# Optimization experiments

Measured on AMD Instinct MI355X. Metric: run time of the kernel, lower is better.

## Reference

```python
import jax, jax.numpy as jnp
import numpy as np
import math

SHIFTS = (1, 2, 4, 8)
EPS_IN = 1e-5  # InstanceNorm2d eps
EPS_BN = 1e-5  # BatchNorm2d eps

def _eight_shifts(x, d):
    # Reproduces DATrans.feature_padding: 8 reflection-padded shifted views.
    H, W = x.shape[-2], x.shape[-1]
    def p(rt, rb, cl, cr):
        return jnp.pad(x, ((0, 0), (0, 0), (rt, rb), (cl, cr)), mode='reflect')
    return [
        p(d, 0, d, 0)[..., :H, :W],   # left-top
        p(d, 0, 0, 0)[..., :H, :],    # center-top
        p(d, 0, 0, d)[..., :H, d:],   # right-top
        p(0, 0, d, 0)[..., :, :W],    # left-center
        p(0, 0, 0, d)[..., :, d:],    # right-center
        p(0, d, d, 0)[..., d:, :W],   # left-bottom
        p(0, d, 0, 0)[..., d:, :],    # center-bottom
        p(0, d, 0, d)[..., d:, d:],   # right-bottom
    ]

def _l2n(x):
    # torch F.normalize(dim=-1, eps=1e-12)
    return x / jnp.maximum(jnp.linalg.norm(x, axis=-1, keepdims=True), 1e-12)

def setup_inputs() -> dict:
    key = jax.random.key(0)
    ks = jax.random.split(key, 9)
    B, Cin, H, W = 4, 16, 256, 256
    heads, hidden, NL, Cout = 4, 16, 8, 16
    tra = heads * hidden
    cen = jax.random.normal(ks[0], (B, Cin, H, W), jnp.float32)
    q_w = jax.random.normal(ks[1], (heads, hidden, Cin), jnp.float32) / np.sqrt(Cin).astype(np.float32)
    k_w = jax.random.normal(ks[2], (heads, hidden * NL, Cin * NL), jnp.float32) / np.sqrt(Cin * NL).astype(np.float32)
    v_w = jax.random.normal(ks[3], (heads, hidden * NL, Cin * NL), jnp.float32) / np.sqrt(Cin * NL).astype(np.float32)
    out_w = jax.random.normal(ks[4], (Cout, tra), jnp.float32) / np.sqrt(tra).astype(np.float32)
    bn_gamma = jax.random.uniform(ks[5], (Cout,), jnp.float32) + 0.5
    bn_beta = jax.random.normal(ks[6], (Cout,), jnp.float32) * 0.1
    bn_mean = jax.random.normal(ks[7], (Cout,), jnp.float32) * 0.1
    bn_var = jax.random.uniform(ks[8], (Cout,), jnp.float32) + 0.5
    return dict(cen=cen, q_w=q_w, k_w=k_w, v_w=v_w, out_w=out_w,
                bn_gamma=bn_gamma, bn_beta=bn_beta, bn_mean=bn_mean, bn_var=bn_var)

def reference(cen, q_w, k_w, v_w, out_w, bn_gamma, bn_beta, bn_mean, bn_var):
    b, Cin, H, W = cen.shape
    area = H * W
    heads = len(SHIFTS)
    qs, ksl, vsl = [], [], []
    for i, d in enumerate(SHIFTS):  # small fixed loop over heads
        sur = jnp.concatenate([s - cen for s in _eight_shifts(cen, d)], axis=1)  # [b, 8*Cin, H, W]
        ksl.append(jnp.einsum('oc,bchw->bohw', k_w[i], sur))  # 1x1 conv, no bias
        vsl.append(jnp.einsum('oc,bchw->bohw', v_w[i], sur))
        qs.append(jnp.einsum('oc,bchw->bohw', q_w[i], cen))
    # torch stack(dim=2).view(b, heads, -1, area) on contiguous tensor == stack+reshape
    K = jnp.stack(ksl, axis=2).reshape(b, heads, -1, area)  # [b, heads, 8*hid, area]
    Q = jnp.stack(qs, axis=2).reshape(b, heads, -1, area)   # [b, heads, hid, area]
    V = jnp.stack(vsl, axis=2).reshape(b, heads, -1, area)
    scores = jnp.einsum('bhca,bhda->bhcd', _l2n(Q), _l2n(K)) / math.sqrt(area)  # [b,h,hid,8*hid]
    # InstanceNorm2d(heads): per (b, head) over last two dims, no affine
    mu = scores.mean(axis=(-2, -1), keepdims=True)
    var = scores.var(axis=(-2, -1), keepdims=True)
    attn = jax.nn.softmax((scores - mu) * jax.lax.rsqrt(var + EPS_IN), axis=-1)
    out = jnp.einsum('bhcd,bhda->bhca', attn, V)  # [b, heads, hid, area]
    tra = out.shape[1] * out.shape[2]
    out = out.reshape(b, tra, H, W)
    out = jnp.einsum('oc,bchw->bohw', out_w, out)  # out_conv 1x1, no bias
    g = bn_gamma[None, :, None, None]
    bta = bn_beta[None, :, None, None]
    m = bn_mean[None, :, None, None]
    v = bn_var[None, :, None, None]
    out = (out - m) * jax.lax.rsqrt(v + EPS_BN) * g + bta  # eval-mode BatchNorm2d
    return jax.nn.relu(out)
```

## Files before the change

kernel.cpp:

```cpp
#include <hip/hip_runtime.h>
#include <math.h>

#define HH 256
#define WW 256
#define AREA 65536
#define CIN 16
#define NS 4
#define CSUR 128
#define NEXT 144
#define NPAIR 45

typedef __attribute__((ext_vector_type(8))) _Float16 f16x8;
typedef __attribute__((ext_vector_type(4))) float f32x4;

__constant__ int c_dy[8] = {-1,-1,-1, 0, 0, 1, 1, 1};
__constant__ int c_dx[8] = {-1, 0, 1,-1, 1,-1, 0, 1};

__device__ constexpr int CTI[NPAIR] = {
    0, 1,1, 2,2,2, 3,3,3,3, 4,4,4,4,4,
    5,5,5,5,5,5, 6,6,6,6,6,6,6, 7,7,7,7,7,7,7,7,
    8,8,8,8,8,8,8,8,8};
__device__ constexpr int CTJ[NPAIR] = {
    0, 0,1, 0,1,2, 0,1,2,3, 0,1,2,3,4,
    0,1,2,3,4,5, 0,1,2,3,4,5,6, 0,1,2,3,4,5,6,7,
    0,1,2,3,4,5,6,7,8};

__device__ __forceinline__ int refl(int v) {
    return v < 0 ? -v : (v > 255 ? 510 - v : v);
}

__device__ __forceinline__ unsigned pkh(float a, float b) {
    auto h2 = __builtin_amdgcn_cvt_pkrtz(a, b);
    return __builtin_bit_cast(unsigned, h2);
}

__device__ __forceinline__ void wph(unsigned* __restrict__ m,
                                    int c, int pxp, int halfk, float a, float b) {
    const int sw = c & 7, gi = halfk * 4 + (pxp >> 2), e = pxp & 3;
    m[c * 32 + ((gi ^ sw) << 2) + e] = pkh(a, b);
}

template <bool FAST>
__device__ __forceinline__ void stage64(unsigned* __restrict__ m,
                                        const float* __restrict__ base,
                                        int y, int x0, int cin, int pxp, int d) {
    constexpr int DY[8] = {-1,-1,-1, 0, 0, 1, 1, 1};
    constexpr int DX[8] = {-1, 0, 1,-1, 1,-1, 0, 1};
    const int xA = x0 + 2 * pxp;
    const int xB = xA + 32;
    const float* rowy = base + y * WW;
    const float2 cA = *(const float2*)(rowy + xA);
    const float2 cB = *(const float2*)(rowy + xB);
    wph(m, cin, pxp, 0, cA.x, cA.y);
    wph(m, cin, pxp, 1, cB.x, cB.y);
#pragma unroll
    for (int kk = 0; kk < 8; ++kk) {
        float2 sA, sB;
        if (FAST) {
            const float* row = base + (y + DY[kk] * d) * WW;
            sA = *(const float2*)(row + xA + DX[kk] * d);
            sB = *(const float2*)(row + xB + DX[kk] * d);
        } else {
            const int ys = refl(y + DY[kk] * d);
            const float* row = base + ys * WW;
            const int off = DX[kk] * d;
            sA.x = row[refl(xA + off)];
            sA.y = row[refl(xA + 1 + off)];
            sB.x = row[refl(xB + off)];
            sB.y = row[refl(xB + 1 + off)];
        }
        const int c = 16 + kk * 16 + cin;
        wph(m, c, pxp, 0, sA.x - cA.x, sA.y - cA.y);
        wph(m, c, pxp, 1, sB.x - cB.x, sB.y - cB.y);
    }
}

__global__ __launch_bounds__(256) void k1_gram(const float* __restrict__ cen,
                                               float* __restrict__ part) {
    const int chunk = blockIdx.x;
    const int s = blockIdx.y;
    const int b = blockIdx.z;
    const int d = 1 << s;
    const int t = threadIdx.x;
    const int lane = t & 63, wid = t >> 6;
    const int lr = lane & 15, lg = lane >> 4;
    const int cin = t >> 4, pxp = t & 15;
    const int y0 = chunk * 4;
    const float* base = cen + ((size_t)b * CIN + cin) * AREA;

    __shared__ unsigned lds[NEXT * 32];

    const int rA = ((lg ^ (lr & 7)) << 2);
    const int rB = (((4 + lg) ^ (lr & 7)) << 2);

    f32x4 acc[12];
#pragma unroll
    for (int i = 0; i < 12; ++i) acc[i] = (f32x4){0.f, 0.f, 0.f, 0.f};

    for (int rd = 0; rd < 16; ++rd) {
        const int y  = y0 + (rd >> 2);
        const int x0 = (rd & 3) * 64;
        if (y >= 8 && y <= 247 && x0 >= 64 && x0 <= 128)
            stage64<true>(lds, base, y, x0, cin, pxp, d);
        else
            stage64<false>(lds, base, y, x0, cin, pxp, d);
        __syncthreads();
        f16x8 fA[9], fB[9];
#pragma unroll
        for (int tt = 0; tt < 9; ++tt) {
            const int rb = (tt * 16 + lr) * 32;
            fA[tt] = __builtin_bit_cast(f16x8, *(const uint4*)(lds + rb + rA));
            fB[tt] = __builtin_bit_cast(f16x8, *(const uint4*)(lds + rb + rB));
        }
        __syncthreads();
#pragma unroll
        for (int p = 0; p < NPAIR; ++p) {
            if ((p & 3) == wid) {
                const int i = CTI[p], j = CTJ[p], a = p >> 2;
                acc[a] = __builtin_amdgcn_mfma_f32_16x16x32_f16(fA[i], fA[j], acc[a], 0, 0, 0);
                acc[a] = __builtin_amdgcn_mfma_f32_16x16x32_f16(fB[i], fB[j], acc[a], 0, 0, 0);
            }
        }
    }

    float* tb = part + (size_t)((chunk & 3) * 16 + b * 4 + s) * 20736;
#pragma unroll
    for (int p = 0; p < NPAIR; ++p) {
        if ((p & 3) == wid) {
            const int gi0 = CTI[p] * 16 + lg * 4;
            const int gj  = CTJ[p] * 16 + lr;
            const f32x4 a = acc[p >> 2];
#pragma unroll
            for (int r = 0; r < 4; ++r)
                atomicAdd(&tb[(gi0 + r) * 144 + gj], a[r]);
        }
    }
}

__global__ __launch_bounds__(256) void kA(const float* __restrict__ part,
                                          const float* __restrict__ q_w,
                                          const float* __restrict__ k_w,
                                          float* __restrict__ A,
                                          float* __restrict__ normK,
                                          float* __restrict__ normQ) {
    const int s = blockIdx.x, b = blockIdx.y, z = blockIdx.z, bs = b * 4 + s;
    const int t = threadIdx.x;
    const int i0 = z * 16;
    __shared__ float Ts[16][148];
    __shared__ float kwS[128][129];
    __shared__ float red[2][128];

    const float* p0 = part + (size_t)(0 * 16 + bs) * 20736;
    const float* p1 = part + (size_t)(1 * 16 + bs) * 20736;
    const float* p2 = part + (size_t)(2 * 16 + bs) * 20736;
    const float* p3 = part + (size_t)(3 * 16 + bs) * 20736;
    for (int e = t; e < 16 * 144; e += 256) {
        const int il = e / 144, j = e - il * 144;
        const int i = i0 + il;
        const int src = (i >= j) ? (i * 144 + j) : (j * 144 + i);
        Ts[il][j] = p0[src] + p1[src] + p2[src] + p3[src];
    }
    if (z >= 1) {
        const float* kws = k_w + (size_t)s * 16384;
        for (int e = t; e < 16384; e += 256)
            kwS[e >> 7][e & 127] = kws[e];
    }
    __syncthreads();

    if (z >= 1) {
        for (int e = t; e < 1024; e += 256) {
            const int il = e >> 6, jq = e & 63;
            const float* qr = q_w + jq * 16;
            float aa = 0.f;
#pragma unroll
            for (int c = 0; c < 16; ++c) aa = fmaf(qr[c], Ts[il][c], aa);
            A[((size_t)bs * 64 + jq) * 128 + (i0 - 16 + il)] = aa;
        }
        const int ck = t & 127, half = t >> 7;
        float accil[16];
#pragma unroll
        for (int il = 0; il < 16; ++il) accil[il] = 0.f;
        for (int j = half * 64; j < half * 64 + 64; ++j) {
            const float kj = kwS[ck][j];
#pragma unroll
            for (int il = 0; il < 16; ++il)
                accil[il] = fmaf(kj, Ts[il][16 + j], accil[il]);
        }
        float prt = 0.f;
#pragma unroll
        for (int il = 0; il < 16; ++il)
            prt = fmaf(kwS[ck][i0 - 16 + il], accil[il], prt);
        red[half][ck] = prt;
        __syncthreads();
        if (t < 128)
            atomicAdd(&normK[(size_t)bs * 128 + t], red[0][t] + red[1][t]);
    } else if (s == 0 && t < 64) {
        float nq = 0.f;
#pragma unroll
        for (int c1 = 0; c1 < 16; ++c1) {
            float ra = 0.f;
#pragma unroll
            for (int c2 = 0; c2 < 16; ++c2)
                ra = fmaf(q_w[t * 16 + c2], Ts[c1][c2], ra);
            nq = fmaf(q_w[t * 16 + c1], ra, nq);
        }
        normQ[b * 64 + t] = nq;
    }
}

__global__ __launch_bounds__(256) void kB(const float* __restrict__ k_w,
                                          const float* __restrict__ v_w,
                                          const float* __restrict__ A,
                                          const float* __restrict__ normK,
                                          const float* __restrict__ normQ,
                                          float* __restrict__ wEff) {
    const int a = blockIdx.x, b = blockIdx.y;
    const int t = threadIdx.x;
    __shared__ float AS[4][16][128];
    __shared__ float kv[4][32][132];
    __shared__ float sc[2048];
    __shared__ float red[256];
    __shared__ float rowred[256];
    __shared__ float rowmax[16], rowsum[16];
    __shared__ float s_mu, s_rs;

    for (int idx = t; idx < 8192; idx += 256) {
        const int sk = idx >> 11, rr = (idx >> 7) & 15, cp = idx & 127;
        const int jq = (rr & 3) * 16 + 4 * a + (rr >> 2);
        AS[sk][rr][cp] = A[((size_t)(b * 4 + sk) * 64 + jq) * 128 + cp];
    }
    for (int idx = t; idx < 16384; idx += 256) {
        const int sk = idx >> 12, ckl = (idx >> 7) & 31, cp = idx & 127;
        kv[sk][ckl][cp] = k_w[((size_t)sk * 128 + 32 * a + ckl) * 128 + cp];
    }
    __syncthreads();
    for (int e = t; e < 2048; e += 256) {
        const int r = e >> 7, dd = e & 127;
        const int sk = dd & 3, ckl = dd >> 2;
        const float4* Ar = (const float4*)(&AS[sk][r][0]);
        const float4* kr = (const float4*)(&kv[sk][ckl][0]);
        float4 pv = {0.f, 0.f, 0.f, 0.f};
#pragma unroll 8
        for (int jj = 0; jj < 32; ++jj) {
            const float4 h = Ar[jj], k4 = kr[jj];
            pv.x = fmaf(h.x, k4.x, pv.x);
            pv.y = fmaf(h.y, k4.y, pv.y);
            pv.z = fmaf(h.z, k4.z, pv.z);
            pv.w = fmaf(h.w, k4.w, pv.w);
        }
        const float dot = pv.x + pv.y + pv.z + pv.w;
        const int jq = (r & 3) * 16 + 4 * a + (r >> 2);
        const float qn = fmaxf(sqrtf(fmaxf(normQ[b * 64 + jq], 0.f)), 1e-12f);
        const float kn = fmaxf(sqrtf(fmaxf(normK[(size_t)(b * 4 + sk) * 128 + 32 * a + ckl], 0.f)), 1e-12f);
        sc[e] = dot / (qn * kn * 256.0f);
    }
    __syncthreads();
    for (int idx = t; idx < 16384; idx += 256) {
        const int sk = idx >> 12, m = (idx >> 7) & 31, cp = idx & 127;
        kv[sk][m][cp] = v_w[((size_t)sk * 128 + 32 * a + m) * 128 + cp];
    }
    {
        float p = 0.f;
        for (int e = t; e < 2048; e += 256) p += sc[e];
        red[t] = p; __syncthreads();
        for (int off = 128; off > 0; off >>= 1) {
            if (t < off) red[t] += red[t + off];
            __syncthreads();
        }
        if (t == 0) s_mu = red[0] * (1.f / 2048.f);
        __syncthreads();
    }
    {
        const float mu = s_mu;
        float p = 0.f;
        for (int e = t; e < 2048; e += 256) { const float z = sc[e] - mu; p += z * z; }
        red[t] = p; __syncthreads();
        for (int off = 128; off > 0; off >>= 1) {
            if (t < off) red[t] += red[t + off];
            __syncthreads();
        }
        if (t == 0) s_rs = rsqrtf(red[0] * (1.f / 2048.f) + 1e-5f);
        __syncthreads();
    }
    const float mu = s_mu, rs = s_rs;
    const int r = t >> 4, l = t & 15;
    {
        float m = -1e30f;
#pragma unroll
        for (int j = 0; j < 8; ++j) {
            const float z = (sc[r * 128 + l + j * 16] - mu) * rs;
            m = fmaxf(m, z);
        }
        rowred[t] = m; __syncthreads();
        if (l == 0) {
            float m2 = rowred[r * 16];
            for (int j = 1; j < 16; ++j) m2 = fmaxf(m2, rowred[r * 16 + j]);
            rowmax[r] = m2;
        }
        __syncthreads();
    }
    {
        float p = 0.f;
#pragma unroll
        for (int j = 0; j < 8; ++j) {
            const float z = (sc[r * 128 + l + j * 16] - mu) * rs;
            p += expf(z - rowmax[r]);
        }
        rowred[t] = p; __syncthreads();
        if (l == 0) {
            float p2 = 0.f;
            for (int j = 0; j < 16; ++j) p2 += rowred[r * 16 + j];
            rowsum[r] = p2;
        }
        __syncthreads();
    }
    {
        float vals[8];
#pragma unroll
        for (int j = 0; j < 8; ++j) {
            const float z = (sc[r * 128 + l + j * 16] - mu) * rs;
            vals[j] = expf(z - rowmax[r]) / rowsum[r];
        }
        __syncthreads();
#pragma unroll
        for (int j = 0; j < 8; ++j) sc[r * 128 + l + j * 16] = vals[j];
        __syncthreads();
    }
    for (int e = t; e < 8192; e += 256) {
        const int sk = e >> 11, r2 = (e >> 7) & 15, cp = e & 127;
        float w = 0.f;
#pragma unroll
        for (int m = 0; m < 32; ++m)
            w = fmaf(sc[r2 * 128 + 4 * m + sk], kv[sk][m][cp], w);
        wEff[((size_t)(b * 4 + sk) * 64 + (a * 16 + r2)) * 128 + cp] = w;
    }
}

__global__ __launch_bounds__(256) void k2c(const float* __restrict__ out_w,
                                           const float* __restrict__ bn_gamma,
                                           const float* __restrict__ bn_var,
                                           const float* __restrict__ wEff,
                                           float* __restrict__ wFinal) {
    const int s = blockIdx.x, b = blockIdx.y;
    const int t = threadIdx.x;
    __shared__ float we[64][128];
    for (int idx = t; idx < 8192; idx += 256) {
        const int j = idx >> 7, cp = idx & 127;
        we[j][cp] = wEff[((size_t)(b * 4 + s) * 64 + j) * 128 + cp];
    }
    __syncthreads();
    for (int e = t; e < 2048; e += 256) {
        const int o = e >> 7, cp = e & 127;
        float w = 0.f;
#pragma unroll 16
        for (int j = 0; j < 64; ++j)
            w = fmaf(out_w[o * 64 + j], we[j][cp], w);
        const float scale = bn_gamma[o] * rsqrtf(bn_var[o] + 1e-5f);
        wFinal[((size_t)(b * 4 + s) * 16 + o) * 128 + cp] = w * scale;
    }
}

__global__ __launch_bounds__(256) void k3_out(const float* __restrict__ cen,
                                              const float* __restrict__ wFinal,
                                              const float* __restrict__ bn_gamma,
                                              const float* __restrict__ bn_beta,
                                              const float* __restrict__ bn_mean,
                                              const float* __restrict__ bn_var,
                                              float* __restrict__ out) {
    const int by = blockIdx.x;
    const int b  = blockIdx.y;
    const int t  = threadIdx.x;
    __shared__ __align__(16) float wf[NS * CSUR * 16];
    __shared__ __align__(16) float wc[16 * 16];

    for (int e = t; e < NS * CSUR * 16; e += 256) {
        const int s = e >> 11, cp = (e >> 4) & 127, o = e & 15;
        wf[e] = wFinal[((size_t)(b * NS + s) * 16 + o) * CSUR + cp];
    }
    __syncthreads();
    {
        const int cin = t >> 4, o = t & 15;
        float sum = 0.f;
#pragma unroll
        for (int s = 0; s < NS; ++s)
#pragma unroll
            for (int k = 0; k < 8; ++k)
                sum += wf[(s * CSUR + k * 16 + cin) * 16 + o];
        wc[cin * 16 + o] = sum;
    }
    __syncthreads();

    const int x0 = t & 127;
    const int x1 = x0 + 128;
    const int y  = by * 2 + (t >> 7);
    const float* cb = cen + (size_t)b * CIN * AREA;

    float acc0[16], acc1[16];
#pragma unroll
    for (int o = 0; o < 16; ++o) { acc0[o] = 0.f; acc1[o] = 0.f; }

    for (int s = 0; s < NS; ++s) {
        const int d = 1 << s;
        for (int k = 0; k < 8; ++k) {
            const int ry  = refl(y + c_dy[k] * d);
            const int rx0 = refl(x0 + c_dx[k] * d);
            const int rx1 = refl(x1 + c_dx[k] * d);
            const float* crow = cb + ry * WW;
#pragma unroll
            for (int cin = 0; cin < 16; ++cin) {
                const float v0 = crow[cin * AREA + rx0];
                const float v1 = crow[cin * AREA + rx1];
                const float4* w4 = reinterpret_cast<const float4*>(&wf[(s * CSUR + k * 16 + cin) * 16]);
#pragma unroll
                for (int oq = 0; oq < 4; ++oq) {
                    const float4 w = w4[oq];
                    acc0[oq*4+0] = fmaf(w.x, v0, acc0[oq*4+0]); acc1[oq*4+0] = fmaf(w.x, v1, acc1[oq*4+0]);
                    acc0[oq*4+1] = fmaf(w.y, v0, acc0[oq*4+1]); acc1[oq*4+1] = fmaf(w.y, v1, acc1[oq*4+1]);
                    acc0[oq*4+2] = fmaf(w.z, v0, acc0[oq*4+2]); acc1[oq*4+2] = fmaf(w.z, v1, acc1[oq*4+2]);
                    acc0[oq*4+3] = fmaf(w.w, v0, acc0[oq*4+3]); acc1[oq*4+3] = fmaf(w.w, v1, acc1[oq*4+3]);
                }
            }
        }
    }
    {
        const float* crow = cb + y * WW;
#pragma unroll
        for (int cin = 0; cin < 16; ++cin) {
            const float v0 = crow[cin * AREA + x0];
            const float v1 = crow[cin * AREA + x1];
            const float4* w4 = reinterpret_cast<const float4*>(&wc[cin * 16]);
#pragma unroll
            for (int oq = 0; oq < 4; ++oq) {
                const float4 w = w4[oq];
                acc0[oq*4+0] = fmaf(-w.x, v0, acc0[oq*4+0]); acc1[oq*4+0] = fmaf(-w.x, v1, acc1[oq*4+0]);
                acc0[oq*4+1] = fmaf(-w.y, v0, acc0[oq*4+1]); acc1[oq*4+1] = fmaf(-w.y, v1, acc1[oq*4+1]);
                acc0[oq*4+2] = fmaf(-w.z, v0, acc0[oq*4+2]); acc1[oq*4+2] = fmaf(-w.z, v1, acc1[oq*4+2]);
                acc0[oq*4+3] = fmaf(-w.w, v0, acc0[oq*4+3]); acc1[oq*4+3] = fmaf(-w.w, v1, acc1[oq*4+3]);
            }
        }
    }
#pragma unroll
    for (int o = 0; o < 16; ++o) {
        const float scale = bn_gamma[o] * rsqrtf(bn_var[o] + 1e-5f);
        const float bias  = bn_beta[o] - bn_mean[o] * scale;
        const float r0 = fmaxf(acc0[o] + bias, 0.f);
        const float r1 = fmaxf(acc1[o] + bias, 0.f);
        out[((size_t)(b * 16 + o) * HH + y) * WW + x0] = r0;
        out[((size_t)(b * 16 + o) * HH + y) * WW + x1] = r1;
    }
}

extern "C" void kernel_launch(void* const* d_in, const int* in_sizes, int n_in,
                              void* d_out, int out_size, void* d_ws, size_t ws_size,
                              hipStream_t stream) {
    const float* cen      = (const float*)d_in[0];
    const float* q_w      = (const float*)d_in[1];
    const float* k_w      = (const float*)d_in[2];
    const float* v_w      = (const float*)d_in[3];
    const float* out_w    = (const float*)d_in[4];
    const float* bn_gamma = (const float*)d_in[5];
    const float* bn_beta  = (const float*)d_in[6];
    const float* bn_mean  = (const float*)d_in[7];
    const float* bn_var   = (const float*)d_in[8];
    float* out = (float*)d_out;

    char* ws = (char*)d_ws;
    const size_t PART_BYTES  = (size_t)4 * 16 * 20736 * 4;
    const size_t NK_BYTES    = (size_t)16 * 128 * 4;
    const size_t A_BYTES     = (size_t)16 * 64 * 128 * 4;
    const size_t NQ_BYTES    = (size_t)4 * 64 * 4;
    const size_t WEFF_BYTES  = (size_t)16 * 64 * 128 * 4;

    float* part  = (float*)(ws);
    float* normK = (float*)(ws + PART_BYTES);
    float* A     = (float*)(ws + PART_BYTES + NK_BYTES);
    float* normQ = (float*)(ws + PART_BYTES + NK_BYTES + A_BYTES);
    float* wEff  = (float*)(ws + PART_BYTES + NK_BYTES + A_BYTES + NQ_BYTES);
    float* wFin  = (float*)(ws + PART_BYTES + NK_BYTES + A_BYTES + NQ_BYTES + WEFF_BYTES);

    (void)hipMemsetAsync(part, 0, PART_BYTES + NK_BYTES, stream);
    k1_gram<<<dim3(64, 4, 4), 256, 0, stream>>>(cen, part);
    kA<<<dim3(4, 4, 9), 256, 0, stream>>>(part, q_w, k_w, A, normK, normQ);
    kB<<<dim3(4, 4), 256, 0, stream>>>(k_w, v_w, A, normK, normQ, wEff);
    k2c<<<dim3(4, 4), 256, 0, stream>>>(out_w, bn_gamma, bn_var, wEff, wFin);
    k3_out<<<dim3(128, 4), 256, 0, stream>>>(cen, wFin, bn_gamma, bn_beta,
                                             bn_mean, bn_var, out);
}
```

Baseline: 260.1 us.

## Double-buffer LDS staging in gram kernel and split score computation into separate kernel

The gram kernel now stages the next 64-pixel tile into a second LDS buffer while MFMAs run on the current one, which drops one barrier per iteration and lets global loads overlap with compute. Separately, the score dot products that kB did in only 16 blocks move into a new k2s kernel launched with 64 blocks, which reads k_w directly from global memory and writes scores to workspace. kB then only loads those scores. This adds a kernel launch and a workspace round-trip but spreads the small serial stage across more CUs, and the extra LDS buffer may lower occupancy of the gram kernel.

After: 264.0 us. Within noise of the previous version (+1.5%).

```diff
diff --git a/kernel.cpp b/kernel.cpp
--- a/kernel.cpp
+++ b/kernel.cpp
@@ -88,7 +88,7 @@
     const int y0 = chunk * 4;
     const float* base = cen + ((size_t)b * CIN + cin) * AREA;
 
-    __shared__ unsigned lds[NEXT * 32];
+    __shared__ unsigned lds[2][NEXT * 32];
 
     const int rA = ((lg ^ (lr & 7)) << 2);
     const int rB = (((4 + lg) ^ (lr & 7)) << 2);
@@ -97,22 +97,26 @@
 #pragma unroll
     for (int i = 0; i < 12; ++i) acc[i] = (f32x4){0.f, 0.f, 0.f, 0.f};
 
+    stage64<false>(lds[0], base, y0, 0, cin, pxp, d);
+    __syncthreads();
+
     for (int rd = 0; rd < 16; ++rd) {
-        const int y  = y0 + (rd >> 2);
-        const int x0 = (rd & 3) * 64;
-        if (y >= 8 && y <= 247 && x0 >= 64 && x0 <= 128)
-            stage64<true>(lds, base, y, x0, cin, pxp, d);
-        else
-            stage64<false>(lds, base, y, x0, cin, pxp, d);
-        __syncthreads();
+        const unsigned* m = lds[rd & 1];
         f16x8 fA[9], fB[9];
 #pragma unroll
         for (int tt = 0; tt < 9; ++tt) {
             const int rb = (tt * 16 + lr) * 32;
-            fA[tt] = __builtin_bit_cast(f16x8, *(const uint4*)(lds + rb + rA));
-            fB[tt] = __builtin_bit_cast(f16x8, *(const uint4*)(lds + rb + rB));
-        }
-        __syncthreads();
+            fA[tt] = __builtin_bit_cast(f16x8, *(const uint4*)(m + rb + rA));
+            fB[tt] = __builtin_bit_cast(f16x8, *(const uint4*)(m + rb + rB));
+        }
+        if (rd + 1 < 16) {
+            const int y  = y0 + ((rd + 1) >> 2);
+            const int x0 = ((rd + 1) & 3) * 64;
+            if (y >= 8 && y <= 247 && x0 >= 64 && x0 <= 128)
+                stage64<true>(lds[(rd + 1) & 1], base, y, x0, cin, pxp, d);
+            else
+                stage64<false>(lds[(rd + 1) & 1], base, y, x0, cin, pxp, d);
+        }
 #pragma unroll
         for (int p = 0; p < NPAIR; ++p) {
             if ((p & 3) == wid) {
@@ -121,6 +125,7 @@
                 acc[a] = __builtin_amdgcn_mfma_f32_16x16x32_f16(fB[i], fB[j], acc[a], 0, 0, 0);
             }
         }
+        __syncthreads();
     }
 
     float* tb = part + (size_t)((chunk & 3) * 16 + b * 4 + s) * 20736;
@@ -208,37 +213,26 @@
     }
 }
 
-__global__ __launch_bounds__(256) void kB(const float* __restrict__ k_w,
-                                          const float* __restrict__ v_w,
-                                          const float* __restrict__ A,
-                                          const float* __restrict__ normK,
-                                          const float* __restrict__ normQ,
-                                          float* __restrict__ wEff) {
-    const int a = blockIdx.x, b = blockIdx.y;
+__global__ __launch_bounds__(256) void k2s(const float* __restrict__ k_w,
+                                           const float* __restrict__ A,
+                                           const float* __restrict__ normK,
+                                           const float* __restrict__ normQ,
+                                           float* __restrict__ scWs) {
+    const int a = blockIdx.x, b = blockIdx.y, rq = blockIdx.z;
     const int t = threadIdx.x;
-    __shared__ float AS[4][16][128];
-    __shared__ float kv[4][32][132];
-    __shared__ float sc[2048];
-    __shared__ float red[256];
-    __shared__ float rowred[256];
-    __shared__ float rowmax[16], rowsum[16];
-    __shared__ float s_mu, s_rs;
-
-    for (int idx = t; idx < 8192; idx += 256) {
-        const int sk = idx >> 11, rr = (idx >> 7) & 15, cp = idx & 127;
-        const int jq = (rr & 3) * 16 + 4 * a + (rr >> 2);
-        AS[sk][rr][cp] = A[((size_t)(b * 4 + sk) * 64 + jq) * 128 + cp];
-    }
-    for (int idx = t; idx < 16384; idx += 256) {
-        const int sk = idx >> 12, ckl = (idx >> 7) & 31, cp = idx & 127;
-        kv[sk][ckl][cp] = k_w[((size_t)sk * 128 + 32 * a + ckl) * 128 + cp];
-    }
-    __syncthreads();
+    __shared__ float AS[16][132];
     for (int e = t; e < 2048; e += 256) {
-        const int r = e >> 7, dd = e & 127;
-        const int sk = dd & 3, ckl = dd >> 2;
-        const float4* Ar = (const float4*)(&AS[sk][r][0]);
-        const float4* kr = (const float4*)(&kv[sk][ckl][0]);
+        const int row = e >> 7, cp = e & 127;
+        const int sk = row >> 2, i = row & 3;
+        const int jq = i * 16 + 4 * a + rq;
+        AS[row][cp] = A[((size_t)(b * 4 + sk) * 64 + jq) * 128 + cp];
+    }
+    __syncthreads();
+    for (int e = t; e < 512; e += 256) {
+        const int sk = e >> 7, i = (e >> 5) & 3, ckl = e & 31;
+        const int jq = i * 16 + 4 * a + rq;
+        const float4* Ar = (const float4*)(&AS[sk * 4 + i][0]);
+        const float4* kr = (const float4*)(k_w + ((size_t)sk * 128 + 32 * a + ckl) * 128);
         float4 pv = {0.f, 0.f, 0.f, 0.f};
 #pragma unroll 8
         for (int jj = 0; jj < 32; ++jj) {
@@ -249,16 +243,33 @@
             pv.w = fmaf(h.w, k4.w, pv.w);
         }
         const float dot = pv.x + pv.y + pv.z + pv.w;
-        const int jq = (r & 3) * 16 + 4 * a + (r >> 2);
         const float qn = fmaxf(sqrtf(fmaxf(normQ[b * 64 + jq], 0.f)), 1e-12f);
         const float kn = fmaxf(sqrtf(fmaxf(normK[(size_t)(b * 4 + sk) * 128 + 32 * a + ckl], 0.f)), 1e-12f);
-        sc[e] = dot / (qn * kn * 256.0f);
-    }
-    __syncthreads();
+        const int r = rq * 4 + i;
+        scWs[((size_t)(b * 4 + a)) * 2048 + r * 128 + 4 * ckl + sk] =
+            dot / (qn * kn * 256.0f);
+    }
+}
+
+__global__ __launch_bounds__(256) void kB(const float* __restrict__ v_w,
+                                          const float* __restrict__ scWs,
+                                          float* __restrict__ wEff) {
+    const int a = blockIdx.x, b = blockIdx.y;
+    const int t = threadIdx.x;
+    __shared__ float kv[4][32][132];
+    __shared__ float sc[2048];
+    __shared__ float red[256];
+    __shared__ float rowred[256];
+    __shared__ float rowmax[16], rowsum[16];
+    __shared__ float s_mu, s_rs;
+
+    for (int idx = t; idx < 2048; idx += 256)
+        sc[idx] = scWs[((size_t)(b * 4 + a)) * 2048 + idx];
     for (int idx = t; idx < 16384; idx += 256) {
         const int sk = idx >> 12, m = (idx >> 7) & 31, cp = idx & 127;
         kv[sk][m][cp] = v_w[((size_t)sk * 128 + 32 * a + m) * 128 + cp];
     }
+    __syncthreads();
     {
         float p = 0.f;
         for (int e = t; e < 2048; e += 256) p += sc[e];
@@ -469,19 +480,22 @@
     const size_t NK_BYTES    = (size_t)16 * 128 * 4;
     const size_t A_BYTES     = (size_t)16 * 64 * 128 * 4;
     const size_t NQ_BYTES    = (size_t)4 * 64 * 4;
+    const size_t SC_BYTES    = (size_t)16 * 2048 * 4;
     const size_t WEFF_BYTES  = (size_t)16 * 64 * 128 * 4;
 
     float* part  = (float*)(ws);
     float* normK = (float*)(ws + PART_BYTES);
     float* A     = (float*)(ws + PART_BYTES + NK_BYTES);
     float* normQ = (float*)(ws + PART_BYTES + NK_BYTES + A_BYTES);
-    float* wEff  = (float*)(ws + PART_BYTES + NK_BYTES + A_BYTES + NQ_BYTES);
-    float* wFin  = (float*)(ws + PART_BYTES + NK_BYTES + A_BYTES + NQ_BYTES + WEFF_BYTES);
+    float* scWs  = (float*)(ws + PART_BYTES + NK_BYTES + A_BYTES + NQ_BYTES);
+    float* wEff  = (float*)(ws + PART_BYTES + NK_BYTES + A_BYTES + NQ_BYTES + SC_BYTES);
+    float* wFin  = (float*)(ws + PART_BYTES + NK_BYTES + A_BYTES + NQ_BYTES + SC_BYTES + WEFF_BYTES);
 
     (void)hipMemsetAsync(part, 0, PART_BYTES + NK_BYTES, stream);
     k1_gram<<<dim3(64, 4, 4), 256, 0, stream>>>(cen, part);
     kA<<<dim3(4, 4, 9), 256, 0, stream>>>(part, q_w, k_w, A, normK, normQ);
-    kB<<<dim3(4, 4), 256, 0, stream>>>(k_w, v_w, A, normK, normQ, wEff);
+    k2s<<<dim3(4, 4, 4), 256, 0, stream>>>(k_w, A, normK, normQ, scWs);
+    kB<<<dim3(4, 4), 256, 0, stream>>>(v_w, scWs, wEff);
     k2c<<<dim3(4, 4), 256, 0, stream>>>(out_w, bn_gamma, bn_var, wEff, wFin);
     k3_out<<<dim3(128, 4), 256, 0, stream>>>(cen, wFin, bn_gamma, bn_beta,
                                              bn_mean, bn_var, out);
```
